# Performance work log

Measured on AMD Instinct MI355X. Metric: run time of the kernel, lower is better.

## Reference

```python
import jax, jax.numpy as jnp
import numpy as np

NUM_HEADS = 16
EPS = 1e-6  # torch LayerNorm default is 1e-5; module uses nn.LayerNorm default
LN_EPS = 1e-5


def layer_norm(x, w, b, eps=LN_EPS):
    # normalize over last dim (head_dim), matching infer_layer_norm
    mu = jnp.mean(x, axis=-1, keepdims=True)
    xc = x - mu
    var = jnp.mean(xc * xc, axis=-1, keepdims=True)
    return xc / jnp.sqrt(var + eps) * w + b


def setup_inputs() -> dict:
    key = jax.random.key(0)
    ks = jax.random.split(key, 4)
    B, N, C = 2, 4096, 1024
    H = NUM_HEADS
    D = C // H
    x = jax.random.normal(ks[0], (B, N, C), dtype=jnp.float32)
    qkv_w = jax.random.normal(ks[1], (3 * C, C), dtype=jnp.float32) * (C ** -0.5)
    qkv_b = jax.random.normal(ks[2], (3 * C,), dtype=jnp.float32) * 0.02
    q_norm_w = jnp.ones((D,), dtype=jnp.float32)
    q_norm_b = jnp.zeros((D,), dtype=jnp.float32)
    k_norm_w = jnp.ones((D,), dtype=jnp.float32)
    k_norm_b = jnp.zeros((D,), dtype=jnp.float32)
    proj_w = jax.random.normal(ks[3], (C, C), dtype=jnp.float32) * (C ** -0.5)
    proj_b = jnp.zeros((C,), dtype=jnp.float32)
    return {"x": x, "qkv_w": qkv_w, "qkv_b": qkv_b,
            "q_norm_w": q_norm_w, "q_norm_b": q_norm_b,
            "k_norm_w": k_norm_w, "k_norm_b": k_norm_b,
            "proj_w": proj_w, "proj_b": proj_b}


def reference(x, qkv_w, qkv_b, q_norm_w, q_norm_b, k_norm_w, k_norm_b, proj_w, proj_b):
    B, N, C = x.shape
    H = NUM_HEADS
    D = C // H
    scale = D ** -0.5
    # QKV projection: torch Linear uses y = x @ W^T + b
    qkv = x @ qkv_w.T + qkv_b                      # [B,N,3C]
    qkv = qkv.reshape(B, N, 3, H, D).transpose(2, 0, 3, 1, 4)  # [3,B,H,N,D]
    q, k, v = qkv[0], qkv[1], qkv[2]
    # per-head qk layernorm
    q = layer_norm(q, q_norm_w, q_norm_b)
    k = layer_norm(k, k_norm_w, k_norm_b)
    # scaled dot product attention
    attn = jnp.einsum('bhqd,bhkd->bhqk', q * scale, k)
    attn = jax.nn.softmax(attn, axis=-1)
    out = jnp.einsum('bhqk,bhkd->bhqd', attn, v)   # [B,H,N,D]
    out = out.transpose(0, 2, 1, 3).reshape(B, N, C)
    return out @ proj_w.T + proj_b
```

## Files before the change

kernel.cpp:

```cpp
#include <hip/hip_runtime.h>
#include <hip/hip_bf16.h>

#define NB 2
#define NN 4096
#define NC 1024
#define NH 16
#define ND 64
#define NM (NB*NN)
#define NK 1024
#define J_QKV 3072
#define QSCALE 0.18033688011112042f

typedef unsigned short u16;
typedef unsigned int   u32;
typedef __attribute__((ext_vector_type(8)))  __bf16 bf16x8;
typedef __attribute__((ext_vector_type(4)))  float  f32x4;
typedef __attribute__((ext_vector_type(16))) float  f32x16;

__device__ __forceinline__ u16 f2bf(float f) {
    unsigned int i = __builtin_bit_cast(unsigned int, f);
    unsigned int lsb = (i >> 16) & 1u;
    i += 0x7fffu + lsb;
    return (u16)(i >> 16);
}
__device__ __forceinline__ float fast_exp2(float x) {
#if __has_builtin(__builtin_amdgcn_exp2f)
    return __builtin_amdgcn_exp2f(x);
#else
    return exp2f(x);
#endif
}
__device__ __forceinline__ u32 pkbf(float a, float b) {
    u32 r;
    asm("v_cvt_pk_bf16_f32 %0, %1, %2" : "=v"(r) : "v"(a), "v"(b));
    return r;
}
typedef struct { u32 x, y; } u32pair;
__device__ __forceinline__ u32pair swap32(u32 a, u32 b) {
#if __has_builtin(__builtin_amdgcn_permlane32_swap)
    auto r = __builtin_amdgcn_permlane32_swap((int)a, (int)b, false, false);
    u32pair o; o.x = (u32)r[0]; o.y = (u32)r[1]; return o;
#else
    const bool hi = (threadIdx.x & 32) != 0;
    u32 as = (u32)__shfl_xor((int)a, 32);
    u32 bs = (u32)__shfl_xor((int)b, 32);
    u32pair o; o.x = hi ? bs : a; o.y = hi ? b : as; return o;
#endif
}

__device__ __forceinline__ void glds16(const u16* g, u16* l) {
    __builtin_amdgcn_global_load_lds(
        (const __attribute__((address_space(1))) u32*)g,
        (__attribute__((address_space(3))) u32*)l, 16, 0, 0);
}

__global__ __launch_bounds__(256) void cvt_bf16(
    const float* __restrict__ in, u16* __restrict__ out)
{
    const size_t i = ((size_t)blockIdx.x * 256 + threadIdx.x) * 8;
    const float4 a = *(const float4*)(in + i);
    const float4 b = *(const float4*)(in + i + 4);
    union { u16 h[8]; uint4 v; } u;
    u.h[0] = f2bf(a.x); u.h[1] = f2bf(a.y); u.h[2] = f2bf(a.z); u.h[3] = f2bf(a.w);
    u.h[4] = f2bf(b.x); u.h[5] = f2bf(b.y); u.h[6] = f2bf(b.z); u.h[7] = f2bf(b.w);
    *(uint4*)(out + i) = u.v;
}

template<int MODE>
__global__ __launch_bounds__(256) void gemm_nt(
    const u16* __restrict__ A, const u16* __restrict__ W,
    const float* __restrict__ bias,
    const float* __restrict__ qw, const float* __restrict__ qb,
    const float* __restrict__ kw, const float* __restrict__ kb,
    void* __restrict__ outv)
{
    __shared__ __align__(16) u16 As[128][32];
    __shared__ __align__(16) u16 Bs[128][32];
    const int t = threadIdx.x;
    const int w = t >> 6, lane = t & 63;
    const int jb = blockIdx.x * 128;
    const int m0 = blockIdx.y * 128;
    const int wr = (w >> 1) * 64, wc = (w & 1) * 64;
    const int srow = t >> 2, skc = (t & 3) * 8;
    const u16* ap0 = A + (size_t)(m0 + srow) * NK + skc;
    const u16* ap1 = ap0 + (size_t)64 * NK;
    const u16* wp0 = W + (size_t)(jb + srow) * NK + skc;
    const u16* wp1 = wp0 + (size_t)64 * NK;
    u16* as0 = &As[srow][skc];      u16* as1 = &As[srow + 64][skc];
    u16* bs0 = &Bs[srow][skc];      u16* bs1 = &Bs[srow + 64][skc];
    const int fm = lane & 15, fk = 8 * (lane >> 4);
    f32x4 acc[4][4];
    #pragma unroll
    for (int i = 0; i < 4; ++i)
        #pragma unroll
        for (int j = 0; j < 4; ++j) acc[i][j] = (f32x4){0.f, 0.f, 0.f, 0.f};

    for (int kt = 0; kt < NK / 32; ++kt) {
        const int ko = kt * 32;
        glds16(ap0 + ko, as0);
        glds16(ap1 + ko, as1);
        glds16(wp0 + ko, bs0);
        glds16(wp1 + ko, bs1);
        __syncthreads();
        bf16x8 af[4], bfr[4];
        #pragma unroll
        for (int i = 0; i < 4; ++i) af[i]  = *(const bf16x8*)&As[wr + 16 * i + fm][fk];
        #pragma unroll
        for (int j = 0; j < 4; ++j) bfr[j] = *(const bf16x8*)&Bs[wc + 16 * j + fm][fk];
        #pragma unroll
        for (int i = 0; i < 4; ++i)
            #pragma unroll
            for (int j = 0; j < 4; ++j)
                acc[i][j] = __builtin_amdgcn_mfma_f32_16x16x32_bf16(af[i], bfr[j], acc[i][j], 0, 0, 0);
        __syncthreads();
    }
    const int c16 = lane & 15;
    float bv[4];
    #pragma unroll
    for (int j = 0; j < 4; ++j) bv[j] = bias[jb + wc + 16 * j + c16];
    #pragma unroll
    for (int i = 0; i < 4; ++i)
        #pragma unroll
        for (int j = 0; j < 4; ++j)
            #pragma unroll
            for (int r = 0; r < 4; ++r) acc[i][j][r] += bv[j];
    if (MODE == 0) {
        const int s = jb >> 10;
        if (s < 2) {
            const float* lw = s ? kw : qw;
            const float* lb = s ? kb : qb;
            float lwv[4], lbv[4];
            #pragma unroll
            for (int j = 0; j < 4; ++j) {
                lwv[j] = lw[16 * j + c16]; lbv[j] = lb[16 * j + c16];
            }
            #pragma unroll
            for (int i = 0; i < 4; ++i)
                #pragma unroll
                for (int r = 0; r < 4; ++r) {
                    float sum = acc[i][0][r] + acc[i][1][r] + acc[i][2][r] + acc[i][3][r];
                    #pragma unroll
                    for (int off = 1; off < 16; off <<= 1) sum += __shfl_xor(sum, off);
                    const float mu = sum * (1.0f / 64.0f);
                    float v2 = 0.f;
                    #pragma unroll
                    for (int j = 0; j < 4; ++j) { const float dd = acc[i][j][r] - mu; v2 += dd * dd; }
                    #pragma unroll
                    for (int off = 1; off < 16; off <<= 1) v2 += __shfl_xor(v2, off);
                    const float rstd = rsqrtf(v2 * (1.0f / 64.0f) + 1e-5f);
                    #pragma unroll
                    for (int j = 0; j < 4; ++j) {
                        float y = (acc[i][j][r] - mu) * rstd * lwv[j] + lbv[j];
                        if (s == 0) y *= QSCALE;
                        acc[i][j][r] = y;
                    }
                }
        }
        u16* out = (u16*)outv;
        const int r0 = 4 * (lane >> 4);
        #pragma unroll
        for (int j = 0; j < 4; ++j) {
            const int col = jb + wc + 16 * j + c16;
            const int ss = col >> 10, hh = (col >> 6) & 15, d = col & 63;
            #pragma unroll
            for (int i = 0; i < 4; ++i)
                #pragma unroll
                for (int r = 0; r < 4; ++r) {
                    const int row = m0 + wr + 16 * i + r0 + r;
                    const int b = row >> 12, n = row & 4095;
                    out[((((size_t)ss * NB + b) * NH + hh) * NN + n) * ND + d] = f2bf(acc[i][j][r]);
                }
        }
    } else {
        float* out = (float*)outv;
        const int r0 = 4 * (lane >> 4);
        #pragma unroll
        for (int i = 0; i < 4; ++i)
            #pragma unroll
            for (int r = 0; r < 4; ++r) {
                const int row = m0 + wr + 16 * i + r0 + r;
                #pragma unroll
                for (int j = 0; j < 4; ++j)
                    out[(size_t)row * NC + jb + wc + 16 * j + c16] = acc[i][j][r];
            }
    }
}

__global__ __launch_bounds__(256, 2) void attn_mfma(
    const u16* __restrict__ qkv, u16* __restrict__ aout)
{
    __shared__ __align__(16) u16 Ks[64][72];
    __shared__ __align__(16) u16 Vt[64][72];
    const int bid  = blockIdx.x;
    const int qblk = bid & 15;
    const int bh   = bid >> 4;
    const int b = bh >> 4, hh = bh & 15;
    const size_t plane = (size_t)NB * NH * NN * ND;
    const size_t base  = ((size_t)(b * NH + hh)) * NN * ND;
    const u16* qp = qkv + base;
    const u16* kp = qkv + plane + base;
    const u16* vp = qkv + 2 * plane + base;
    const int t = threadIdx.x, w = t >> 6, lane = t & 63;
    const int half = lane >> 5, m32 = lane & 31;
    const int q0 = qblk * 256 + 64 * w;

    bf16x8 qf[2][4];
    #pragma unroll
    for (int s = 0; s < 2; ++s) {
        const u16* qrow = qp + (size_t)(q0 + 32 * s + m32) * ND + 8 * half;
        #pragma unroll
        for (int kt = 0; kt < 4; ++kt) qf[s][kt] = *(const bf16x8*)(qrow + 16 * kt);
    }
    f32x16 O[2][2], z;
    #pragma unroll
    for (int r = 0; r < 16; ++r) { O[0][0][r] = 0.f; O[0][1][r] = 0.f;
                                   O[1][0][r] = 0.f; O[1][1][r] = 0.f; z[r] = 0.f; }
    float lpart[2] = {0.f, 0.f};

    const int dgK = 16 * w;
    const int kp2 = t & 31, dgV = (t >> 5) * 8;
    const u16* ksrc = kp + (size_t)lane * ND + dgK;
    const u16* vsrc = vp + (size_t)(2 * kp2) * ND + dgV;

    uint4 kr0, kr1, vre, vro;
    kr0 = *(const uint4*)(ksrc);
    kr1 = *(const uint4*)(ksrc + 8);
    vre = *(const uint4*)(vsrc);
    vro = *(const uint4*)(vsrc + ND);
    {
        *(uint4*)&Ks[lane][dgK]     = kr0;
        *(uint4*)&Ks[lane][dgK + 8] = kr1;
        const u32* ew = (const u32*)&vre;
        const u32* ow = (const u32*)&vro;
        #pragma unroll
        for (int d = 0; d < 4; ++d) {
            u32 lo = __builtin_amdgcn_perm(ow[d], ew[d], 0x05040100u);
            u32 hi = __builtin_amdgcn_perm(ow[d], ew[d], 0x07060302u);
            *(u32*)&Vt[dgV + 2 * d][2 * kp2]     = lo;
            *(u32*)&Vt[dgV + 2 * d + 1][2 * kp2] = hi;
        }
    }
    __syncthreads();

    for (int kb = 0; kb < NN / 64; ++kb) {
        const bool more = (kb + 1) < (NN / 64);
        if (more) {
            const u16* ks2 = ksrc + (size_t)(kb + 1) * 64 * ND;
            kr0 = *(const uint4*)ks2;
            kr1 = *(const uint4*)(ks2 + 8);
            const u16* vs2 = vsrc + (size_t)(kb + 1) * 64 * ND;
            vre = *(const uint4*)vs2;
            vro = *(const uint4*)(vs2 + ND);
        }
        f32x16 sT[2][2];
        __builtin_amdgcn_s_setprio(1);
        {
            bf16x8 k0 = *(const bf16x8*)&Ks[m32][8 * half];
            bf16x8 k1 = *(const bf16x8*)&Ks[32 + m32][8 * half];
            sT[0][0] = __builtin_amdgcn_mfma_f32_32x32x16_bf16(k0, qf[0][0], z, 0, 0, 0);
            sT[0][1] = __builtin_amdgcn_mfma_f32_32x32x16_bf16(k1, qf[0][0], z, 0, 0, 0);
            sT[1][0] = __builtin_amdgcn_mfma_f32_32x32x16_bf16(k0, qf[1][0], z, 0, 0, 0);
            sT[1][1] = __builtin_amdgcn_mfma_f32_32x32x16_bf16(k1, qf[1][0], z, 0, 0, 0);
        }
        #pragma unroll
        for (int kt = 1; kt < 4; ++kt) {
            bf16x8 k0 = *(const bf16x8*)&Ks[m32][16 * kt + 8 * half];
            bf16x8 k1 = *(const bf16x8*)&Ks[32 + m32][16 * kt + 8 * half];
            sT[0][0] = __builtin_amdgcn_mfma_f32_32x32x16_bf16(k0, qf[0][kt], sT[0][0], 0, 0, 0);
            sT[0][1] = __builtin_amdgcn_mfma_f32_32x32x16_bf16(k1, qf[0][kt], sT[0][1], 0, 0, 0);
            sT[1][0] = __builtin_amdgcn_mfma_f32_32x32x16_bf16(k0, qf[1][kt], sT[1][0], 0, 0, 0);
            sT[1][1] = __builtin_amdgcn_mfma_f32_32x32x16_bf16(k1, qf[1][kt], sT[1][1], 0, 0, 0);
        }
        __builtin_amdgcn_s_setprio(0);
        union W8 { u32 wd[4]; bf16x8 f; } pa[2][4];
        #pragma unroll
        for (int s = 0; s < 2; ++s) {
            float ss0 = 0.f, ss1 = 0.f;
            #pragma unroll
            for (int kh = 0; kh < 2; ++kh) {
                float p[16];
                #pragma unroll
                for (int r = 0; r < 16; ++r) p[r] = fast_exp2(sT[s][kh][r]);
                #pragma unroll
                for (int r = 0; r < 8; ++r) { ss0 += p[r]; ss1 += p[8 + r]; }
                u32 c[4][2];
                #pragma unroll
                for (int g = 0; g < 4; ++g) {
                    c[g][0] = pkbf(p[4 * g + 0], p[4 * g + 1]);
                    c[g][1] = pkbf(p[4 * g + 2], p[4 * g + 3]);
                }
                #pragma unroll
                for (int par = 0; par < 2; ++par) {
                    u32pair wA = swap32(c[2 * par][0], c[2 * par + 1][0]);
                    u32pair wB = swap32(c[2 * par][1], c[2 * par + 1][1]);
                    const int kt = 2 * kh + par;
                    pa[s][kt].wd[0] = wA.x;
                    pa[s][kt].wd[1] = wB.x;
                    pa[s][kt].wd[2] = wA.y;
                    pa[s][kt].wd[3] = wB.y;
                }
            }
            lpart[s] += ss0 + ss1;
        }
        __builtin_amdgcn_s_setprio(1);
        #pragma unroll
        for (int kt = 0; kt < 4; ++kt) {
            bf16x8 v0 = *(const bf16x8*)&Vt[m32][16 * kt + 8 * half];
            bf16x8 v1 = *(const bf16x8*)&Vt[32 + m32][16 * kt + 8 * half];
            O[0][0] = __builtin_amdgcn_mfma_f32_32x32x16_bf16(pa[0][kt].f, v0, O[0][0], 0, 0, 0);
            O[0][1] = __builtin_amdgcn_mfma_f32_32x32x16_bf16(pa[0][kt].f, v1, O[0][1], 0, 0, 0);
            O[1][0] = __builtin_amdgcn_mfma_f32_32x32x16_bf16(pa[1][kt].f, v0, O[1][0], 0, 0, 0);
            O[1][1] = __builtin_amdgcn_mfma_f32_32x32x16_bf16(pa[1][kt].f, v1, O[1][1], 0, 0, 0);
        }
        __builtin_amdgcn_s_setprio(0);
        if (more) {
            __syncthreads();
            *(uint4*)&Ks[lane][dgK]     = kr0;
            *(uint4*)&Ks[lane][dgK + 8] = kr1;
            const u32* ew = (const u32*)&vre;
            const u32* ow = (const u32*)&vro;
            #pragma unroll
            for (int d = 0; d < 4; ++d) {
                u32 lo = __builtin_amdgcn_perm(ow[d], ew[d], 0x05040100u);
                u32 hi = __builtin_amdgcn_perm(ow[d], ew[d], 0x07060302u);
                *(u32*)&Vt[dgV + 2 * d][2 * kp2]     = lo;
                *(u32*)&Vt[dgV + 2 * d + 1][2 * kp2] = hi;
            }
            __syncthreads();
        }
    }
    #pragma unroll
    for (int s = 0; s < 2; ++s) {
        const float tot = lpart[s] + __shfl_xor(lpart[s], 32);
        #pragma unroll
        for (int r = 0; r < 16; ++r) {
            const int qq = (r & 3) + 8 * (r >> 2) + 4 * half;
            const float inv = 1.0f / __shfl(tot, qq);
            const int row = q0 + 32 * s + qq;
            u16* dst = aout + ((size_t)(b * NN + row)) * NC + hh * 64;
            dst[m32]      = f2bf(O[s][0][r] * inv);
            dst[32 + m32] = f2bf(O[s][1][r] * inv);
        }
    }
}

extern "C" void kernel_launch(void* const* d_in, const int* in_sizes, int n_in,
                              void* d_out, int out_size, void* d_ws, size_t ws_size,
                              hipStream_t stream) {
    const float* x     = (const float*)d_in[0];
    const float* qkv_w = (const float*)d_in[1];
    const float* qkv_b = (const float*)d_in[2];
    const float* q_nw  = (const float*)d_in[3];
    const float* q_nb  = (const float*)d_in[4];
    const float* k_nw  = (const float*)d_in[5];
    const float* k_nb  = (const float*)d_in[6];
    const float* p_w   = (const float*)d_in[7];
    const float* p_b   = (const float*)d_in[8];
    float* out = (float*)d_out;
    u16* qkv    = (u16*)d_ws;
    u16* x_bf   = qkv + (size_t)3 * NB * NH * NN * ND;
    u16* attn_o = x_bf;
    u16* w_bf   = x_bf + (size_t)NM * NC;
    u16* pw_bf  = w_bf + (size_t)J_QKV * NK;

    cvt_bf16<<<(NM * NC) / 2048, 256, 0, stream>>>(x, x_bf);
    cvt_bf16<<<(J_QKV * NK) / 2048, 256, 0, stream>>>(qkv_w, w_bf);
    cvt_bf16<<<(NC * NK) / 2048, 256, 0, stream>>>(p_w, pw_bf);

    gemm_nt<0><<<dim3(J_QKV / 128, NM / 128), 256, 0, stream>>>(
        x_bf, w_bf, qkv_b, q_nw, q_nb, k_nw, k_nb, qkv);
    attn_mfma<<<NB * NH * (NN / 256), 256, 0, stream>>>(qkv, attn_o);
    gemm_nt<1><<<dim3(NC / 128, NM / 128), 256, 0, stream>>>(
        attn_o, pw_bf, p_b, q_nw, q_nb, k_nw, k_nb, out);
}
```

Measured before the change: 359.4 us.

## Double-buffer K/V tiles in LDS and split attention into two sub-tile passes

Ks and Vt become two-slot LDS buffers, so the next K/V tile is written into the other slot and one of the two barriers per iteration is dropped. The QK^T, softmax and PV work is also reordered per 32-row sub-tile instead of interleaving both, which lets the exp work of one sub-tile overlap the MFMAs of the other. LDS use doubles to about 36 KB per block, which may limit occupancy with two blocks per CU. Per-sub-tile scheduling may also shorten the MFMA chains the compiler can interleave.

```diff
diff --git a/kernel.cpp b/kernel.cpp
--- a/kernel.cpp
+++ b/kernel.cpp
@@ -189,8 +189,8 @@
 __global__ __launch_bounds__(256, 2) void attn_mfma(
     const u16* __restrict__ qkv, u16* __restrict__ aout)
 {
-    __shared__ __align__(16) u16 Ks[64][72];
-    __shared__ __align__(16) u16 Vt[64][72];
+    __shared__ __align__(16) u16 Ks[2][64][72];
+    __shared__ __align__(16) u16 Vt[2][64][72];
     const int bid  = blockIdx.x;
     const int qblk = bid & 15;
     const int bh   = bid >> 4;
@@ -228,21 +228,24 @@
     vre = *(const uint4*)(vsrc);
     vro = *(const uint4*)(vsrc + ND);
     {
-        *(uint4*)&Ks[lane][dgK]     = kr0;
-        *(uint4*)&Ks[lane][dgK + 8] = kr1;
+        *(uint4*)&Ks[0][lane][dgK]     = kr0;
+        *(uint4*)&Ks[0][lane][dgK + 8] = kr1;
         const u32* ew = (const u32*)&vre;
         const u32* ow = (const u32*)&vro;
         #pragma unroll
         for (int d = 0; d < 4; ++d) {
             u32 lo = __builtin_amdgcn_perm(ow[d], ew[d], 0x05040100u);
             u32 hi = __builtin_amdgcn_perm(ow[d], ew[d], 0x07060302u);
-            *(u32*)&Vt[dgV + 2 * d][2 * kp2]     = lo;
-            *(u32*)&Vt[dgV + 2 * d + 1][2 * kp2] = hi;
+            *(u32*)&Vt[0][dgV + 2 * d][2 * kp2]     = lo;
+            *(u32*)&Vt[0][dgV + 2 * d + 1][2 * kp2] = hi;
         }
     }
     __syncthreads();
 
+    union W8 { u32 wd[4]; bf16x8 f; };
+
     for (int kb = 0; kb < NN / 64; ++kb) {
+        const int cur = kb & 1, nxt = cur ^ 1;
         const bool more = (kb + 1) < (NN / 64);
         if (more) {
             const u16* ks2 = ksrc + (size_t)(kb + 1) * 64 * ND;
@@ -252,35 +255,43 @@
             vre = *(const uint4*)vs2;
             vro = *(const uint4*)(vs2 + ND);
         }
-        f32x16 sT[2][2];
+        f32x16 sT0[2], sT1[2];
         __builtin_amdgcn_s_setprio(1);
         {
-            bf16x8 k0 = *(const bf16x8*)&Ks[m32][8 * half];
-            bf16x8 k1 = *(const bf16x8*)&Ks[32 + m32][8 * half];
-            sT[0][0] = __builtin_amdgcn_mfma_f32_32x32x16_bf16(k0, qf[0][0], z, 0, 0, 0);
-            sT[0][1] = __builtin_amdgcn_mfma_f32_32x32x16_bf16(k1, qf[0][0], z, 0, 0, 0);
-            sT[1][0] = __builtin_amdgcn_mfma_f32_32x32x16_bf16(k0, qf[1][0], z, 0, 0, 0);
-            sT[1][1] = __builtin_amdgcn_mfma_f32_32x32x16_bf16(k1, qf[1][0], z, 0, 0, 0);
+            bf16x8 k0 = *(const bf16x8*)&Ks[cur][m32][8 * half];
+            bf16x8 k1 = *(const bf16x8*)&Ks[cur][32 + m32][8 * half];
+            sT0[0] = __builtin_amdgcn_mfma_f32_32x32x16_bf16(k0, qf[0][0], z, 0, 0, 0);
+            sT0[1] = __builtin_amdgcn_mfma_f32_32x32x16_bf16(k1, qf[0][0], z, 0, 0, 0);
         }
         #pragma unroll
         for (int kt = 1; kt < 4; ++kt) {
-            bf16x8 k0 = *(const bf16x8*)&Ks[m32][16 * kt + 8 * half];
-            bf16x8 k1 = *(const bf16x8*)&Ks[32 + m32][16 * kt + 8 * half];
-            sT[0][0] = __builtin_amdgcn_mfma_f32_32x32x16_bf16(k0, qf[0][kt], sT[0][0], 0, 0, 0);
-            sT[0][1] = __builtin_amdgcn_mfma_f32_32x32x16_bf16(k1, qf[0][kt], sT[0][1], 0, 0, 0);
-            sT[1][0] = __builtin_amdgcn_mfma_f32_32x32x16_bf16(k0, qf[1][kt], sT[1][0], 0, 0, 0);
-            sT[1][1] = __builtin_amdgcn_mfma_f32_32x32x16_bf16(k1, qf[1][kt], sT[1][1], 0, 0, 0);
+            bf16x8 k0 = *(const bf16x8*)&Ks[cur][m32][16 * kt + 8 * half];
+            bf16x8 k1 = *(const bf16x8*)&Ks[cur][32 + m32][16 * kt + 8 * half];
+            sT0[0] = __builtin_amdgcn_mfma_f32_32x32x16_bf16(k0, qf[0][kt], sT0[0], 0, 0, 0);
+            sT0[1] = __builtin_amdgcn_mfma_f32_32x32x16_bf16(k1, qf[0][kt], sT0[1], 0, 0, 0);
+        }
+        {
+            bf16x8 k0 = *(const bf16x8*)&Ks[cur][m32][8 * half];
+            bf16x8 k1 = *(const bf16x8*)&Ks[cur][32 + m32][8 * half];
+            sT1[0] = __builtin_amdgcn_mfma_f32_32x32x16_bf16(k0, qf[1][0], z, 0, 0, 0);
+            sT1[1] = __builtin_amdgcn_mfma_f32_32x32x16_bf16(k1, qf[1][0], z, 0, 0, 0);
+        }
+        #pragma unroll
+        for (int kt = 1; kt < 4; ++kt) {
+            bf16x8 k0 = *(const bf16x8*)&Ks[cur][m32][16 * kt + 8 * half];
+            bf16x8 k1 = *(const bf16x8*)&Ks[cur][32 + m32][16 * kt + 8 * half];
+            sT1[0] = __builtin_amdgcn_mfma_f32_32x32x16_bf16(k0, qf[1][kt], sT1[0], 0, 0, 0);
+            sT1[1] = __builtin_amdgcn_mfma_f32_32x32x16_bf16(k1, qf[1][kt], sT1[1], 0, 0, 0);
         }
         __builtin_amdgcn_s_setprio(0);
-        union W8 { u32 wd[4]; bf16x8 f; } pa[2][4];
-        #pragma unroll
-        for (int s = 0; s < 2; ++s) {
+        W8 pa0[4], pa1[4];
+        {
             float ss0 = 0.f, ss1 = 0.f;
             #pragma unroll
             for (int kh = 0; kh < 2; ++kh) {
                 float p[16];
                 #pragma unroll
-                for (int r = 0; r < 16; ++r) p[r] = fast_exp2(sT[s][kh][r]);
+                for (int r = 0; r < 16; ++r) p[r] = fast_exp2(sT0[kh][r]);
                 #pragma unroll
                 for (int r = 0; r < 8; ++r) { ss0 += p[r]; ss1 += p[8 + r]; }
                 u32 c[4][2];
@@ -294,37 +305,71 @@
                     u32pair wA = swap32(c[2 * par][0], c[2 * par + 1][0]);
                     u32pair wB = swap32(c[2 * par][1], c[2 * par + 1][1]);
                     const int kt = 2 * kh + par;
-                    pa[s][kt].wd[0] = wA.x;
-                    pa[s][kt].wd[1] = wB.x;
-                    pa[s][kt].wd[2] = wA.y;
-                    pa[s][kt].wd[3] = wB.y;
+                    pa0[kt].wd[0] = wA.x;
+                    pa0[kt].wd[1] = wB.x;
+                    pa0[kt].wd[2] = wA.y;
+                    pa0[kt].wd[3] = wB.y;
                 }
             }
-            lpart[s] += ss0 + ss1;
+            lpart[0] += ss0 + ss1;
         }
         __builtin_amdgcn_s_setprio(1);
         #pragma unroll
         for (int kt = 0; kt < 4; ++kt) {
-            bf16x8 v0 = *(const bf16x8*)&Vt[m32][16 * kt + 8 * half];
-            bf16x8 v1 = *(const bf16x8*)&Vt[32 + m32][16 * kt + 8 * half];
-            O[0][0] = __builtin_amdgcn_mfma_f32_32x32x16_bf16(pa[0][kt].f, v0, O[0][0], 0, 0, 0);
-            O[0][1] = __builtin_amdgcn_mfma_f32_32x32x16_bf16(pa[0][kt].f, v1, O[0][1], 0, 0, 0);
-            O[1][0] = __builtin_amdgcn_mfma_f32_32x32x16_bf16(pa[1][kt].f, v0, O[1][0], 0, 0, 0);
-            O[1][1] = __builtin_amdgcn_mfma_f32_32x32x16_bf16(pa[1][kt].f, v1, O[1][1], 0, 0, 0);
+            bf16x8 v0 = *(const bf16x8*)&Vt[cur][m32][16 * kt + 8 * half];
+            bf16x8 v1 = *(const bf16x8*)&Vt[cur][32 + m32][16 * kt + 8 * half];
+            O[0][0] = __builtin_amdgcn_mfma_f32_32x32x16_bf16(pa0[kt].f, v0, O[0][0], 0, 0, 0);
+            O[0][1] = __builtin_amdgcn_mfma_f32_32x32x16_bf16(pa0[kt].f, v1, O[0][1], 0, 0, 0);
+        }
+        __builtin_amdgcn_s_setprio(0);
+        {
+            float ss0 = 0.f, ss1 = 0.f;
+            #pragma unroll
+            for (int kh = 0; kh < 2; ++kh) {
+                float p[16];
+                #pragma unroll
+                for (int r = 0; r < 16; ++r) p[r] = fast_exp2(sT1[kh][r]);
+                #pragma unroll
+                for (int r = 0; r < 8; ++r) { ss0 += p[r]; ss1 += p[8 + r]; }
+                u32 c[4][2];
+                #pragma unroll
+                for (int g = 0; g < 4; ++g) {
+                    c[g][0] = pkbf(p[4 * g + 0], p[4 * g + 1]);
+                    c[g][1] = pkbf(p[4 * g + 2], p[4 * g + 3]);
+                }
+                #pragma unroll
+                for (int par = 0; par < 2; ++par) {
+                    u32pair wA = swap32(c[2 * par][0], c[2 * par + 1][0]);
+                    u32pair wB = swap32(c[2 * par][1], c[2 * par + 1][1]);
+                    const int kt = 2 * kh + par;
+                    pa1[kt].wd[0] = wA.x;
+                    pa1[kt].wd[1] = wB.x;
+                    pa1[kt].wd[2] = wA.y;
+                    pa1[kt].wd[3] = wB.y;
+                }
+            }
+            lpart[1] += ss0 + ss1;
+        }
+        __builtin_amdgcn_s_setprio(1);
+        #pragma unroll
+        for (int kt = 0; kt < 4; ++kt) {
+            bf16x8 v0 = *(const bf16x8*)&Vt[cur][m32][16 * kt + 8 * half];
+            bf16x8 v1 = *(const bf16x8*)&Vt[cur][32 + m32][16 * kt + 8 * half];
+            O[1][0] = __builtin_amdgcn_mfma_f32_32x32x16_bf16(pa1[kt].f, v0, O[1][0], 0, 0, 0);
+            O[1][1] = __builtin_amdgcn_mfma_f32_32x32x16_bf16(pa1[kt].f, v1, O[1][1], 0, 0, 0);
         }
         __builtin_amdgcn_s_setprio(0);
         if (more) {
-            __syncthreads();
-            *(uint4*)&Ks[lane][dgK]     = kr0;
-            *(uint4*)&Ks[lane][dgK + 8] = kr1;
+            *(uint4*)&Ks[nxt][lane][dgK]     = kr0;
+            *(uint4*)&Ks[nxt][lane][dgK + 8] = kr1;
             const u32* ew = (const u32*)&vre;
             const u32* ow = (const u32*)&vro;
             #pragma unroll
             for (int d = 0; d < 4; ++d) {
                 u32 lo = __builtin_amdgcn_perm(ow[d], ew[d], 0x05040100u);
                 u32 hi = __builtin_amdgcn_perm(ow[d], ew[d], 0x07060302u);
-                *(u32*)&Vt[dgV + 2 * d][2 * kp2]     = lo;
-                *(u32*)&Vt[dgV + 2 * d + 1][2 * kp2] = hi;
+                *(u32*)&Vt[nxt][dgV + 2 * d][2 * kp2]     = lo;
+                *(u32*)&Vt[nxt][dgV + 2 * d + 1][2 * kp2] = hi;
             }
             __syncthreads();
         }
```

Measured after the change: 363.9 us. No clear change (+1.3%).
